# Kernel tuning notes

Measured on AMD Instinct MI355X. Metric: run time of the kernel, lower is better.

## Reference

```python
import jax, jax.numpy as jnp
import numpy as np

B, S, E, H = 4, 2048, 1024, 16
D = E // H
MAX_DIST = 4
LN_EPS = 1e-5


def setup_inputs() -> dict:
    key = jax.random.key(0)
    ks = jax.random.split(key, 12)
    std = 1.0 / np.sqrt(E)
    inp = {
        "x": jax.random.normal(ks[0], (B, S, E), dtype=jnp.float32),
        "distances": jax.random.randint(ks[1], (B, S, S), 0, 5, dtype=jnp.int64),
        "Wq": jax.random.normal(ks[2], (E, E), dtype=jnp.float32) * std,
        "bq": jnp.zeros((E,), dtype=jnp.float32),
        "Wk": jax.random.normal(ks[3], (E, E), dtype=jnp.float32) * std,
        "bk": jnp.zeros((E,), dtype=jnp.float32),
        "Wv": jax.random.normal(ks[4], (E, E), dtype=jnp.float32) * std,
        "bv": jnp.zeros((E,), dtype=jnp.float32),
        "Wo": jax.random.normal(ks[5], (E, E), dtype=jnp.float32) * std,
        "bo": jnp.zeros((E,), dtype=jnp.float32),
        "dist_bias": jax.random.normal(ks[6], (MAX_DIST + 1,), dtype=jnp.float32) * 0.1,
        "ln_g": jnp.ones((E,), dtype=jnp.float32),
        "ln_b": jnp.zeros((E,), dtype=jnp.float32),
    }
    return inp


def _layernorm(y, g, b):
    mu = jnp.mean(y, axis=-1, keepdims=True)
    var = jnp.mean(jnp.square(y - mu), axis=-1, keepdims=True)
    return (y - mu) * jax.lax.rsqrt(var + LN_EPS) * g + b


def reference(x, distances, Wq, bq, Wk, bk, Wv, bv, Wo, bo, dist_bias, ln_g, ln_b):
    scale = 1.0 / np.sqrt(D)
    # projections (torch Linear: x @ W.T + b), split into heads -> [B,H,S,D]
    def heads(y):
        return y.reshape(B, S, H, D).transpose(0, 2, 1, 3)
    q = heads(x @ Wq.T + bq)
    k = heads(x @ Wk.T + bk)
    v = heads(x @ Wv.T + bv)
    scores = jnp.einsum('bhsd,bhtd->bhst', q, k) * scale  # [B,H,S,S]
    d = jnp.clip(distances, 0, MAX_DIST)
    bias = dist_bias[d]  # [B,S,S] gather from learned table
    scores = scores + bias[:, None, :, :]
    attn = jax.nn.softmax(scores, axis=-1)
    out = jnp.einsum('bhst,bhtd->bhsd', attn, v)
    out = out.transpose(0, 2, 1, 3).reshape(B, S, E)
    out = out @ Wo.T + bo
    return _layernorm(x + out, ln_g, ln_b)
```

## Files before the change

kernel.cpp:

```cpp
#include <hip/hip_runtime.h>
#include <stdint.h>

#define NB 4
#define NS 2048
#define NE 1024
#define NH 16
#define ND 64
#define LN_EPS 1e-5f
#define LN2I 1.44269504089f

typedef __attribute__((ext_vector_type(8))) unsigned short u16x8;
typedef __attribute__((ext_vector_type(4))) unsigned short u16x4;
typedef __attribute__((ext_vector_type(8))) short b16x8;
typedef __attribute__((ext_vector_type(4))) float f32x4;
typedef __attribute__((ext_vector_type(16))) float f32x16;
typedef __attribute__((ext_vector_type(4))) unsigned u32x4;

static __device__ __forceinline__ unsigned short f2bf(float f) {
  unsigned u = __builtin_bit_cast(unsigned, f);
  u += 0x7FFFu + ((u >> 16) & 1u);
  return (unsigned short)(u >> 16);
}
static __device__ __forceinline__ float bf2f(unsigned short h) {
  return __builtin_bit_cast(float, (unsigned)h << 16);
}
static __device__ __forceinline__ float bperm_f(int addr, float v) {
  return __builtin_bit_cast(float,
      __builtin_amdgcn_ds_bpermute(addr, __builtin_bit_cast(int, v)));
}
static __device__ __forceinline__ unsigned cvtpk(float lo, float hi) {
  unsigned r;
  asm("v_cvt_pk_bf16_f32 %0, %1, %2" : "=v"(r) : "v"(lo), "v"(hi));
  return r;
}
static __device__ __forceinline__ void plswap(unsigned &a, unsigned &b) {
  asm("v_permlane32_swap_b32 %0, %1" : "+v"(a), "+v"(b));
}
#if __has_builtin(__builtin_amdgcn_exp2f)
static __device__ __forceinline__ float ex2(float x) { return __builtin_amdgcn_exp2f(x); }
#else
static __device__ __forceinline__ float ex2(float x) { return exp2f(x); }
#endif

static __device__ __forceinline__ void gload16(const unsigned short* gsrc,
                                               unsigned short* ldsbase) {
  __builtin_amdgcn_global_load_lds(
      (__attribute__((address_space(1))) unsigned int*)(uintptr_t)gsrc,
      (__attribute__((address_space(3))) unsigned int*)(uintptr_t)ldsbase,
      16, 0, 0);
}

#define MFMA16(a, b, c) __builtin_amdgcn_mfma_f32_16x16x32_bf16( \
    __builtin_bit_cast(b16x8, a), __builtin_bit_cast(b16x8, b), c, 0, 0, 0)
#define MFMA32(a, b, c) __builtin_amdgcn_mfma_f32_32x32x16_bf16( \
    __builtin_bit_cast(b16x8, a), __builtin_bit_cast(b16x8, b), c, 0, 0, 0)

__global__ void k_cvt(const float* __restrict__ src, unsigned short* __restrict__ dst, int n) {
  int i = (blockIdx.x * 256 + threadIdx.x) * 8;
  if (i >= n) return;
  float4 a = *(const float4*)(src + i);
  float4 b = *(const float4*)(src + i + 4);
  u16x8 o;
  o[0]=f2bf(a.x); o[1]=f2bf(a.y); o[2]=f2bf(a.z); o[3]=f2bf(a.w);
  o[4]=f2bf(b.x); o[5]=f2bf(b.y); o[6]=f2bf(b.z); o[7]=f2bf(b.w);
  *(u16x8*)(dst + i) = o;
}

__global__ void k_cvtw(const float* __restrict__ w0, const float* __restrict__ w1,
                       const float* __restrict__ w2, const float* __restrict__ w3,
                       unsigned short* __restrict__ d0, unsigned short* __restrict__ d1,
                       unsigned short* __restrict__ d2, unsigned short* __restrict__ d3) {
  const int z = blockIdx.y;
  const float* src = (z == 0) ? w0 : (z == 1) ? w1 : (z == 2) ? w2 : w3;
  unsigned short* dst = (z == 0) ? d0 : (z == 1) ? d1 : (z == 2) ? d2 : d3;
  int i = (blockIdx.x * 256 + threadIdx.x) * 8;
  float4 a = *(const float4*)(src + i);
  float4 b = *(const float4*)(src + i + 4);
  u16x8 o;
  o[0]=f2bf(a.x); o[1]=f2bf(a.y); o[2]=f2bf(a.z); o[3]=f2bf(a.w);
  o[4]=f2bf(b.x); o[5]=f2bf(b.y); o[6]=f2bf(b.z); o[7]=f2bf(b.w);
  *(u16x8*)(dst + i) = o;
}

__global__ void k_bias(const int* __restrict__ d, const float* __restrict__ tbl,
                       unsigned short* __restrict__ bias) {
  size_t i = ((size_t)blockIdx.x * 256 + threadIdx.x) * 8;
  int4 a = *(const int4*)(d + i);
  int4 b = *(const int4*)(d + i + 4);
  u16x8 o;
  int v;
  v = a.x; v = v < 0 ? 0 : (v > 4 ? 4 : v); o[0] = f2bf(tbl[v] * LN2I);
  v = a.y; v = v < 0 ? 0 : (v > 4 ? 4 : v); o[1] = f2bf(tbl[v] * LN2I);
  v = a.z; v = v < 0 ? 0 : (v > 4 ? 4 : v); o[2] = f2bf(tbl[v] * LN2I);
  v = a.w; v = v < 0 ? 0 : (v > 4 ? 4 : v); o[3] = f2bf(tbl[v] * LN2I);
  v = b.x; v = v < 0 ? 0 : (v > 4 ? 4 : v); o[4] = f2bf(tbl[v] * LN2I);
  v = b.y; v = v < 0 ? 0 : (v > 4 ? 4 : v); o[5] = f2bf(tbl[v] * LN2I);
  v = b.z; v = v < 0 ? 0 : (v > 4 ? 4 : v); o[6] = f2bf(tbl[v] * LN2I);
  v = b.w; v = v < 0 ? 0 : (v > 4 ? 4 : v); o[7] = f2bf(tbl[v] * LN2I);
  *(u16x8*)(bias + i) = o;
}

__global__ __launch_bounds__(256, 3) void k_qkv(
    const unsigned short* __restrict__ xb,
    const unsigned short* __restrict__ wq, const unsigned short* __restrict__ wk_,
    const unsigned short* __restrict__ wv,
    const float* __restrict__ bq, const float* __restrict__ bk_, const float* __restrict__ bv,
    unsigned short* __restrict__ q, unsigned short* __restrict__ kk,
    unsigned short* __restrict__ vt) {
  __shared__ unsigned short sA[128 * 64];
  __shared__ unsigned short sB[128 * 64];
  const int tid = threadIdx.x;
  const int lane = tid & 63, wid = tid >> 6;
  const int g = lane >> 4, c16 = lane & 15;
  const int wm = wid >> 1, wn = wid & 1;
  const int z = blockIdx.z;
  const unsigned short* w = (z == 0) ? wq : ((z == 1) ? wk_ : wv);
  const float* bias = (z == 0) ? bq : ((z == 1) ? bk_ : bv);
  const int n0 = blockIdx.x * 128, m0 = blockIdx.y * 128;

  f32x4 acc[4][4];
#pragma unroll
  for (int i = 0; i < 4; ++i)
#pragma unroll
    for (int j = 0; j < 4; ++j) acc[i][j] = f32x4{0.f, 0.f, 0.f, 0.f};

  const int crow = lane >> 3, gcol8 = (lane & 7) * 8;

  for (int k0 = 0; k0 < NE; k0 += 64) {
#pragma unroll
    for (int i = 0; i < 4; ++i) {
      int c = wid * 4 + i;
      int row = c * 8 + crow;
      gload16(xb + (size_t)(m0 + row) * NE + k0 + gcol8, &sA[c * 512]);
      gload16(w + (size_t)(n0 + row) * NE + k0 + gcol8, &sB[c * 512]);
    }
    __syncthreads();
#pragma unroll
    for (int dc = 0; dc < 2; ++dc) {
      u16x8 af[4], bf[4];
#pragma unroll
      for (int mt = 0; mt < 4; ++mt)
        af[mt] = *(const u16x8*)(sA + (wm * 64 + mt * 16 + c16) * 64 + dc * 32 + g * 8);
#pragma unroll
      for (int nt = 0; nt < 4; ++nt)
        bf[nt] = *(const u16x8*)(sB + (wn * 64 + nt * 16 + c16) * 64 + dc * 32 + g * 8);
#pragma unroll
      for (int mt = 0; mt < 4; ++mt)
#pragma unroll
        for (int nt = 0; nt < 4; ++nt)
          acc[mt][nt] = MFMA16(af[mt], bf[nt], acc[mt][nt]);
    }
    __syncthreads();
  }

  if (z == 0) {
#pragma unroll
    for (int mt = 0; mt < 4; ++mt)
#pragma unroll
      for (int nt = 0; nt < 4; ++nt) {
        int col = n0 + wn * 64 + nt * 16 + c16;
        float bb = bias[col];
#pragma unroll
        for (int rr = 0; rr < 4; ++rr) {
          int row = m0 + wm * 64 + mt * 16 + g * 4 + rr;
          q[(size_t)row * NE + col] = f2bf(acc[mt][nt][rr] + bb);
        }
      }
  } else if (z == 1) {
#pragma unroll
    for (int mt = 0; mt < 4; ++mt)
#pragma unroll
      for (int nt = 0; nt < 4; ++nt) {
        int col = n0 + wn * 64 + nt * 16 + c16;
        float bb = bias[col];
        int seg = col & ~63, d = col & 63;
#pragma unroll
        for (int rr = 0; rr < 4; ++rr) {
          int row = m0 + wm * 64 + mt * 16 + g * 4 + rr;
          int dsw = (((d >> 3) ^ (row & 7)) << 3) | (d & 7);
          kk[(size_t)row * NE + seg + dsw] = f2bf(acc[mt][nt][rr] + bb);
        }
      }
  } else {
#pragma unroll
    for (int mt = 0; mt < 4; ++mt)
#pragma unroll
      for (int nt = 0; nt < 4; ++nt) {
        int col = n0 + wn * 64 + nt * 16 + c16;
        float bb = bias[col];
        int h = col >> 6, dd = col & 63;
        int grow = m0 + wm * 64 + mt * 16 + g * 4;
        int b = grow >> 11, ss = grow & 2047;
        int ssw = (ss & ~63) | (((((ss >> 3) & 7) ^ (dd & 7)) << 3)) | (ss & 7);
        u16x4 o;
#pragma unroll
        for (int rr = 0; rr < 4; ++rr) o[rr] = f2bf(acc[mt][nt][rr] + bb);
        *(u16x4*)(vt + ((size_t)((b * NH + h) * ND + dd)) * NS + ssw) = o;
      }
  }
}

__global__ __launch_bounds__(256, 4) void k_attn(
    const unsigned short* __restrict__ q, const unsigned short* __restrict__ kk,
    const unsigned short* __restrict__ vt, const unsigned short* __restrict__ bias,
    unsigned short* __restrict__ attn) {
  __shared__ unsigned short sK[2][64 * 64];
  __shared__ unsigned short sV[2][64 * 64];
  const int tid = threadIdx.x, lane = tid & 63, wid = tid >> 6;
  const int c32 = lane & 31, hi = lane >> 5;
  const int flat = blockIdx.x;
  const int kdec = flat >> 3;
  const int h = kdec & 15;
  const int G = (flat & 7) | ((kdec >> 4) << 3);
  const int b = G >> 4, qb = G & 15;
  const int q0 = qb * 128 + wid * 32;
  const size_t qkbase = ((size_t)b * NS) * NE + (size_t)h * ND;
  const size_t vbase = ((size_t)(b * NH + h) * ND) * NS;
  const unsigned short* brow = bias + (size_t)b * NS * NS + (size_t)(q0 + c32) * NS;

  u16x8 qf[4];
#pragma unroll
  for (int dc = 0; dc < 4; ++dc)
    qf[dc] = *(const u16x8*)(q + qkbase + (size_t)(q0 + c32) * NE + dc * 16 + hi * 8);

  f32x16 oa[2];
#pragma unroll
  for (int j = 0; j < 2; ++j)
#pragma unroll
    for (int i = 0; i < 16; ++i) oa[j][i] = 0.f;
  float l = 0.f;

  const int crow = lane >> 3, gcol8 = (lane & 7) * 8;
  const int swz = c32 & 7;

  auto stage = [&](int kt, int ib) {
#pragma unroll
    for (int i = 0; i < 4; ++i) {
      int c = wid * 4 + i;
      if (c < 8)
        gload16(kk + qkbase + (size_t)(kt + c * 8 + crow) * NE + gcol8, &sK[ib][c * 512]);
      else
        gload16(vt + vbase + (size_t)((c - 8) * 8 + crow) * NS + kt + gcol8, &sV[ib][(c - 8) * 512]);
    }
  };

  stage(0, 0);

  for (int kt = 0, it = 0; kt < NS; kt += 64, ++it) {
    __syncthreads();
    if (kt + 64 < NS) stage(kt + 64, (it + 1) & 1);
    const unsigned short* bK = &sK[it & 1][0];
    const unsigned short* bV = &sV[it & 1][0];

#pragma unroll
    for (int ts = 0; ts < 2; ++ts) {
      u16x4 bp[4];
#pragma unroll
      for (int k8 = 0; k8 < 4; ++k8)
        bp[k8] = *(const u16x4*)(brow + kt + ts * 32 + k8 * 8 + 4 * hi);
      f32x16 s;
#pragma unroll
      for (int i = 0; i < 16; ++i) s[i] = 0.f;
      __builtin_amdgcn_s_setprio(1);
#pragma unroll
      for (int dc = 0; dc < 4; ++dc) {
        u16x8 kf = *(const u16x8*)(bK + (ts * 32 + c32) * 64 + (((dc * 2 + hi) ^ swz) << 3));
        s = MFMA32(kf, qf[dc], s);
      }
      __builtin_amdgcn_s_setprio(0);
      float rs = 0.f;
#pragma unroll
      for (int r = 0; r < 16; ++r) {
        float e = ex2(s[r] * (0.125f * LN2I) + bf2f(bp[r >> 2][r & 3]));
        s[r] = e;
        rs += e;
      }
      l += rs;
      unsigned u0 = cvtpk(s[0], s[1]), u1 = cvtpk(s[2], s[3]);
      unsigned u2 = cvtpk(s[4], s[5]), u3 = cvtpk(s[6], s[7]);
      plswap(u0, u2);
      plswap(u1, u3);
      u32x4 pa0 = (u32x4){u0, u1, u2, u3};
      unsigned u4 = cvtpk(s[8], s[9]), u5 = cvtpk(s[10], s[11]);
      unsigned u6 = cvtpk(s[12], s[13]), u7 = cvtpk(s[14], s[15]);
      plswap(u4, u6);
      plswap(u5, u7);
      u32x4 pa1 = (u32x4){u4, u5, u6, u7};
      __builtin_amdgcn_s_setprio(1);
#pragma unroll
      for (int kc2 = 0; kc2 < 2; ++kc2) {
        const int kc = ts * 2 + kc2;
        const u32x4 pak = kc2 ? pa1 : pa0;
#pragma unroll
        for (int dcol = 0; dcol < 2; ++dcol) {
          u16x8 vf = *(const u16x8*)(bV + (dcol * 32 + c32) * 64 + (((kc * 2 + hi) ^ swz) << 3));
          oa[dcol] = MFMA32(pak, vf, oa[dcol]);
        }
      }
      __builtin_amdgcn_s_setprio(0);
    }
  }

  float lt = l + __shfl_xor(l, 32);
  float invl = 1.0f / lt;
#pragma unroll
  for (int r = 0; r < 16; ++r) {
    int qrow = (r & 3) + 8 * (r >> 2) + 4 * hi;
    float inv_r = bperm_f(qrow << 2, invl);
#pragma unroll
    for (int dcol = 0; dcol < 2; ++dcol)
      attn[qkbase + (size_t)(q0 + qrow) * NE + dcol * 32 + c32] = f2bf(oa[dcol][r] * inv_r);
  }
}

__global__ __launch_bounds__(256, 3) void k_proj(
    const unsigned short* __restrict__ a, const unsigned short* __restrict__ w,
    const float* __restrict__ bo, const float* __restrict__ x, float* __restrict__ y) {
  __shared__ unsigned short sA[128 * 64];
  __shared__ unsigned short sB[128 * 64];
  const int tid = threadIdx.x;
  const int lane = tid & 63, wid = tid >> 6;
  const int g = lane >> 4, c16 = lane & 15;
  const int wm = wid >> 1, wn = wid & 1;
  const int n0 = blockIdx.x * 128, m0 = blockIdx.y * 128;

  f32x4 acc[4][4];
#pragma unroll
  for (int i = 0; i < 4; ++i)
#pragma unroll
    for (int j = 0; j < 4; ++j) acc[i][j] = f32x4{0.f, 0.f, 0.f, 0.f};

  const int crow = lane >> 3, gcol8 = (lane & 7) * 8;

  for (int k0 = 0; k0 < NE; k0 += 64) {
#pragma unroll
    for (int i = 0; i < 4; ++i) {
      int c = wid * 4 + i;
      int row = c * 8 + crow;
      gload16(a + (size_t)(m0 + row) * NE + k0 + gcol8, &sA[c * 512]);
      gload16(w + (size_t)(n0 + row) * NE + k0 + gcol8, &sB[c * 512]);
    }
    __syncthreads();
#pragma unroll
    for (int dc = 0; dc < 2; ++dc) {
      u16x8 af[4], bf[4];
#pragma unroll
      for (int mt = 0; mt < 4; ++mt)
        af[mt] = *(const u16x8*)(sA + (wm * 64 + mt * 16 + c16) * 64 + dc * 32 + g * 8);
#pragma unroll
      for (int nt = 0; nt < 4; ++nt)
        bf[nt] = *(const u16x8*)(sB + (wn * 64 + nt * 16 + c16) * 64 + dc * 32 + g * 8);
#pragma unroll
      for (int mt = 0; mt < 4; ++mt)
#pragma unroll
        for (int nt = 0; nt < 4; ++nt)
          acc[mt][nt] = MFMA16(af[mt], bf[nt], acc[mt][nt]);
    }
    __syncthreads();
  }

#pragma unroll
  for (int mt = 0; mt < 4; ++mt)
#pragma unroll
    for (int nt = 0; nt < 4; ++nt) {
      int col = n0 + wn * 64 + nt * 16 + c16;
      float bb = bo[col];
#pragma unroll
      for (int rr = 0; rr < 4; ++rr) {
        int row = m0 + wm * 64 + mt * 16 + g * 4 + rr;
        y[(size_t)row * NE + col] = acc[mt][nt][rr] + bb + x[(size_t)row * NE + col];
      }
    }
}

__global__ void k_ln(const float* __restrict__ y, const float* __restrict__ gg,
                     const float* __restrict__ bb, float* __restrict__ out) {
  const int row = blockIdx.x, tid = threadIdx.x;
  float4 v = *(const float4*)(y + (size_t)row * NE + tid * 4);
  float s = v.x + v.y + v.z + v.w;
  float s2 = v.x * v.x + v.y * v.y + v.z * v.z + v.w * v.w;
#pragma unroll
  for (int off = 1; off < 64; off <<= 1) {
    s += __shfl_xor(s, off);
    s2 += __shfl_xor(s2, off);
  }
  __shared__ float red[8];
  const int wid = tid >> 6, lane = tid & 63;
  if (lane == 0) { red[wid * 2] = s; red[wid * 2 + 1] = s2; }
  __syncthreads();
  s = red[0] + red[2] + red[4] + red[6];
  s2 = red[1] + red[3] + red[5] + red[7];
  float mu = s * (1.0f / NE);
  float var = s2 * (1.0f / NE) - mu * mu;
  float rstd = rsqrtf(var + LN_EPS);
  float4 g4 = *(const float4*)(gg + tid * 4);
  float4 b4 = *(const float4*)(bb + tid * 4);
  float4 o;
  o.x = (v.x - mu) * rstd * g4.x + b4.x;
  o.y = (v.y - mu) * rstd * g4.y + b4.y;
  o.z = (v.z - mu) * rstd * g4.z + b4.z;
  o.w = (v.w - mu) * rstd * g4.w + b4.w;
  *(float4*)(out + (size_t)row * NE + tid * 4) = o;
}

extern "C" void kernel_launch(void* const* d_in, const int* in_sizes, int n_in,
                              void* d_out, int out_size, void* d_ws, size_t ws_size,
                              hipStream_t stream) {
  (void)in_sizes; (void)n_in; (void)out_size; (void)ws_size;
  const float* x = (const float*)d_in[0];
  const int* dist = (const int*)d_in[1];
  const float* Wq = (const float*)d_in[2];
  const float* bq = (const float*)d_in[3];
  const float* Wk = (const float*)d_in[4];
  const float* bk = (const float*)d_in[5];
  const float* Wv = (const float*)d_in[6];
  const float* bv = (const float*)d_in[7];
  const float* Wo = (const float*)d_in[8];
  const float* bo = (const float*)d_in[9];
  const float* tbl = (const float*)d_in[10];
  const float* lng = (const float*)d_in[11];
  const float* lnb = (const float*)d_in[12];
  float* out = (float*)d_out;

  char* ws = (char*)d_ws;
  size_t off = 0;
  auto alloc = [&](size_t bytes) {
    char* p = ws + off;
    off += (bytes + 255) & ~(size_t)255;
    return p;
  };
  unsigned short* xb = (unsigned short*)d_out;
  unsigned short* wqb = (unsigned short*)alloc((size_t)NE * NE * 2);
  unsigned short* wkb = (unsigned short*)alloc((size_t)NE * NE * 2);
  unsigned short* wvb = (unsigned short*)alloc((size_t)NE * NE * 2);
  unsigned short* wob = (unsigned short*)alloc((size_t)NE * NE * 2);
  unsigned short* qq  = (unsigned short*)alloc((size_t)NB * NS * NE * 2);
  unsigned short* kb  = (unsigned short*)alloc((size_t)NB * NS * NE * 2);
  unsigned short* vtb = (unsigned short*)alloc((size_t)NB * NS * NE * 2);
  unsigned short* attn = (unsigned short*)alloc((size_t)NB * NS * NE * 2);
  unsigned short* bias = (unsigned short*)alloc((size_t)NB * NS * NS * 2);
  float* y = out;

  k_cvt<<<NB * NS * NE / 2048, 256, 0, stream>>>(x, xb, NB * NS * NE);
  k_cvtw<<<dim3(NE * NE / 2048, 4), 256, 0, stream>>>(Wq, Wk, Wv, Wo, wqb, wkb, wvb, wob);
  k_bias<<<(NB * NS * NS) / 2048, 256, 0, stream>>>(dist, tbl, bias);
  k_qkv<<<dim3(NE / 128, NB * NS / 128, 3), 256, 0, stream>>>(
      xb, wqb, wkb, wvb, bq, bk, bv, qq, kb, vtb);
  k_attn<<<dim3(NB * (NS / 128) * NH), 256, 0, stream>>>(qq, kb, vtb, bias, attn);
  k_proj<<<dim3(NE / 128, NB * NS / 128), 256, 0, stream>>>(attn, wob, bo, x, y);
  k_ln<<<NB * NS, 256, 0, stream>>>(y, lng, lnb, out);
}
```

Before: 330.5 us.

## Restructure attention inner loop to batch QK MFMAs and prefetch bias tiles

The attention kernel now computes both 32-key score tiles back to back before the softmax. It software-pipelines the global bias loads: the next tile's first half is prefetched into registers during the current iteration, and the second half is loaded early. The PV MFMAs are merged into one loop of four steps. Launch bounds drop from 4 to 3 waves per SIMD to make room for the extra live registers, which trades occupancy for more instruction-level overlap of MFMA, exp and global-load latency.

Result: faster. 315.9 us (-4.4%).

```diff
diff --git a/kernel.cpp b/kernel.cpp
--- a/kernel.cpp
+++ b/kernel.cpp
@@ -200,7 +200,7 @@
   }
 }
 
-__global__ __launch_bounds__(256, 4) void k_attn(
+__global__ __launch_bounds__(256, 3) void k_attn(
     const unsigned short* __restrict__ q, const unsigned short* __restrict__ kk,
     const unsigned short* __restrict__ vt, const unsigned short* __restrict__ bias,
     unsigned short* __restrict__ attn) {
@@ -223,11 +223,9 @@
   for (int dc = 0; dc < 4; ++dc)
     qf[dc] = *(const u16x8*)(q + qkbase + (size_t)(q0 + c32) * NE + dc * 16 + hi * 8);
 
-  f32x16 oa[2];
-#pragma unroll
-  for (int j = 0; j < 2; ++j)
-#pragma unroll
-    for (int i = 0; i < 16; ++i) oa[j][i] = 0.f;
+  f32x16 oa0, oa1;
+#pragma unroll
+  for (int i = 0; i < 16; ++i) { oa0[i] = 0.f; oa1[i] = 0.f; }
   float l = 0.f;
 
   const int crow = lane >> 3, gcol8 = (lane & 7) * 8;
@@ -244,7 +242,11 @@
     }
   };
 
+  u16x4 bp0[4], bp1[4];
   stage(0, 0);
+#pragma unroll
+  for (int k8 = 0; k8 < 4; ++k8)
+    bp0[k8] = *(const u16x4*)(brow + k8 * 8 + 4 * hi);
 
   for (int kt = 0, it = 0; kt < NS; kt += 64, ++it) {
     __syncthreads();
@@ -253,52 +255,76 @@
     const unsigned short* bV = &sV[it & 1][0];
 
 #pragma unroll
-    for (int ts = 0; ts < 2; ++ts) {
-      u16x4 bp[4];
+    for (int k8 = 0; k8 < 4; ++k8)
+      bp1[k8] = *(const u16x4*)(brow + kt + 32 + k8 * 8 + 4 * hi);
+
+    f32x16 s0, s1;
+#pragma unroll
+    for (int i = 0; i < 16; ++i) { s0[i] = 0.f; s1[i] = 0.f; }
+    __builtin_amdgcn_s_setprio(1);
+#pragma unroll
+    for (int dc = 0; dc < 4; ++dc) {
+      u16x8 kf = *(const u16x8*)(bK + c32 * 64 + (((dc * 2 + hi) ^ swz) << 3));
+      s0 = MFMA32(kf, qf[dc], s0);
+    }
+#pragma unroll
+    for (int dc = 0; dc < 4; ++dc) {
+      u16x8 kf = *(const u16x8*)(bK + (32 + c32) * 64 + (((dc * 2 + hi) ^ swz) << 3));
+      s1 = MFMA32(kf, qf[dc], s1);
+    }
+    __builtin_amdgcn_s_setprio(0);
+
+    float rs = 0.f;
+#pragma unroll
+    for (int r = 0; r < 16; ++r) {
+      float e = ex2(s0[r] * (0.125f * LN2I) + bf2f(bp0[r >> 2][r & 3]));
+      s0[r] = e;
+      rs += e;
+    }
+    l += rs;
+    unsigned u0 = cvtpk(s0[0], s0[1]), u1 = cvtpk(s0[2], s0[3]);
+    unsigned u2 = cvtpk(s0[4], s0[5]), u3 = cvtpk(s0[6], s0[7]);
+    plswap(u0, u2); plswap(u1, u3);
+    u32x4 pa0 = (u32x4){u0, u1, u2, u3};
+    unsigned u4 = cvtpk(s0[8], s0[9]), u5 = cvtpk(s0[10], s0[11]);
+    unsigned u6 = cvtpk(s0[12], s0[13]), u7 = cvtpk(s0[14], s0[15]);
+    plswap(u4, u6); plswap(u5, u7);
+    u32x4 pa1 = (u32x4){u4, u5, u6, u7};
+
+    if (kt + 64 < NS) {
 #pragma unroll
       for (int k8 = 0; k8 < 4; ++k8)
-        bp[k8] = *(const u16x4*)(brow + kt + ts * 32 + k8 * 8 + 4 * hi);
-      f32x16 s;
-#pragma unroll
-      for (int i = 0; i < 16; ++i) s[i] = 0.f;
-      __builtin_amdgcn_s_setprio(1);
-#pragma unroll
-      for (int dc = 0; dc < 4; ++dc) {
-        u16x8 kf = *(const u16x8*)(bK + (ts * 32 + c32) * 64 + (((dc * 2 + hi) ^ swz) << 3));
-        s = MFMA32(kf, qf[dc], s);
-      }
-      __builtin_amdgcn_s_setprio(0);
-      float rs = 0.f;
-#pragma unroll
-      for (int r = 0; r < 16; ++r) {
-        float e = ex2(s[r] * (0.125f * LN2I) + bf2f(bp[r >> 2][r & 3]));
-        s[r] = e;
-        rs += e;
-      }
-      l += rs;
-      unsigned u0 = cvtpk(s[0], s[1]), u1 = cvtpk(s[2], s[3]);
-      unsigned u2 = cvtpk(s[4], s[5]), u3 = cvtpk(s[6], s[7]);
-      plswap(u0, u2);
-      plswap(u1, u3);
-      u32x4 pa0 = (u32x4){u0, u1, u2, u3};
-      unsigned u4 = cvtpk(s[8], s[9]), u5 = cvtpk(s[10], s[11]);
-      unsigned u6 = cvtpk(s[12], s[13]), u7 = cvtpk(s[14], s[15]);
-      plswap(u4, u6);
-      plswap(u5, u7);
-      u32x4 pa1 = (u32x4){u4, u5, u6, u7};
-      __builtin_amdgcn_s_setprio(1);
-#pragma unroll
-      for (int kc2 = 0; kc2 < 2; ++kc2) {
-        const int kc = ts * 2 + kc2;
-        const u32x4 pak = kc2 ? pa1 : pa0;
-#pragma unroll
-        for (int dcol = 0; dcol < 2; ++dcol) {
-          u16x8 vf = *(const u16x8*)(bV + (dcol * 32 + c32) * 64 + (((kc * 2 + hi) ^ swz) << 3));
-          oa[dcol] = MFMA32(pak, vf, oa[dcol]);
-        }
-      }
-      __builtin_amdgcn_s_setprio(0);
-    }
+        bp0[k8] = *(const u16x4*)(brow + kt + 64 + k8 * 8 + 4 * hi);
+    }
+
+    rs = 0.f;
+#pragma unroll
+    for (int r = 0; r < 16; ++r) {
+      float e = ex2(s1[r] * (0.125f * LN2I) + bf2f(bp1[r >> 2][r & 3]));
+      s1[r] = e;
+      rs += e;
+    }
+    l += rs;
+    u0 = cvtpk(s1[0], s1[1]); u1 = cvtpk(s1[2], s1[3]);
+    u2 = cvtpk(s1[4], s1[5]); u3 = cvtpk(s1[6], s1[7]);
+    plswap(u0, u2); plswap(u1, u3);
+    u32x4 pa2 = (u32x4){u0, u1, u2, u3};
+    u4 = cvtpk(s1[8], s1[9]); u5 = cvtpk(s1[10], s1[11]);
+    u6 = cvtpk(s1[12], s1[13]); u7 = cvtpk(s1[14], s1[15]);
+    plswap(u4, u6); plswap(u5, u7);
+    u32x4 pa3 = (u32x4){u4, u5, u6, u7};
+
+    __builtin_amdgcn_s_setprio(1);
+#pragma unroll
+    for (int kc = 0; kc < 4; ++kc) {
+      const u32x4 pak = (kc == 0) ? pa0 : (kc == 1) ? pa1 : (kc == 2) ? pa2 : pa3;
+      const int gsl = ((kc * 2 + hi) ^ swz) << 3;
+      u16x8 vf0 = *(const u16x8*)(bV + c32 * 64 + gsl);
+      u16x8 vf1 = *(const u16x8*)(bV + (32 + c32) * 64 + gsl);
+      oa0 = MFMA32(pak, vf0, oa0);
+      oa1 = MFMA32(pak, vf1, oa1);
+    }
+    __builtin_amdgcn_s_setprio(0);
   }
 
   float lt = l + __shfl_xor(l, 32);
@@ -307,9 +333,8 @@
   for (int r = 0; r < 16; ++r) {
     int qrow = (r & 3) + 8 * (r >> 2) + 4 * hi;
     float inv_r = bperm_f(qrow << 2, invl);
-#pragma unroll
-    for (int dcol = 0; dcol < 2; ++dcol)
-      attn[qkbase + (size_t)(q0 + qrow) * NE + dcol * 32 + c32] = f2bf(oa[dcol][r] * inv_r);
+    attn[qkbase + (size_t)(q0 + qrow) * NE + c32] = f2bf(oa0[r] * inv_r);
+    attn[qkbase + (size_t)(q0 + qrow) * NE + 32 + c32] = f2bf(oa1[r] * inv_r);
   }
 }
 
```

## Enlarge attention blocks to 512 threads, prefetch bias, compute row sums via MFMA

Applied to the files above, without the earlier changes.

The attention kernel now runs 8 waves per block covering 256 query rows, so each staged K/V tile in LDS is shared by twice as many waves, and the grid shrinks to match. Distance-bias fragments are double-buffered in registers and prefetched one half-tile ahead to hide global load latency. The softmax denominator is now accumulated with extra MFMAs against a ones vector rather than a scalar add chain plus cross-lane shuffles. The MFMA row sum is taken from bf16-rounded probabilities, which changes numerics slightly, and the larger block may lower occupancy flexibility.

Result: faster. 322.6 us (-2.4%).

```diff
diff --git a/kernel.cpp b/kernel.cpp
--- a/kernel.cpp
+++ b/kernel.cpp
@@ -23,10 +23,6 @@
 }
 static __device__ __forceinline__ float bf2f(unsigned short h) {
   return __builtin_bit_cast(float, (unsigned)h << 16);
-}
-static __device__ __forceinline__ float bperm_f(int addr, float v) {
-  return __builtin_bit_cast(float,
-      __builtin_amdgcn_ds_bpermute(addr, __builtin_bit_cast(int, v)));
 }
 static __device__ __forceinline__ unsigned cvtpk(float lo, float hi) {
   unsigned r;
@@ -200,7 +196,7 @@
   }
 }
 
-__global__ __launch_bounds__(256, 4) void k_attn(
+__global__ __launch_bounds__(512, 2) void k_attn(
     const unsigned short* __restrict__ q, const unsigned short* __restrict__ kk,
     const unsigned short* __restrict__ vt, const unsigned short* __restrict__ bias,
     unsigned short* __restrict__ attn) {
@@ -212,8 +208,8 @@
   const int kdec = flat >> 3;
   const int h = kdec & 15;
   const int G = (flat & 7) | ((kdec >> 4) << 3);
-  const int b = G >> 4, qb = G & 15;
-  const int q0 = qb * 128 + wid * 32;
+  const int b = G >> 3, qb = G & 7;
+  const int q0 = qb * 256 + wid * 32;
   const size_t qkbase = ((size_t)b * NS) * NE + (size_t)h * ND;
   const size_t vbase = ((size_t)(b * NH + h) * ND) * NS;
   const unsigned short* brow = bias + (size_t)b * NS * NS + (size_t)(q0 + c32) * NS;
@@ -223,20 +219,21 @@
   for (int dc = 0; dc < 4; ++dc)
     qf[dc] = *(const u16x8*)(q + qkbase + (size_t)(q0 + c32) * NE + dc * 16 + hi * 8);
 
-  f32x16 oa[2];
-#pragma unroll
-  for (int j = 0; j < 2; ++j)
-#pragma unroll
-    for (int i = 0; i < 16; ++i) oa[j][i] = 0.f;
-  float l = 0.f;
+  u16x8 onesv;
+#pragma unroll
+  for (int i = 0; i < 8; ++i) onesv[i] = 0x3F80;
+
+  f32x16 oa[2], l_acc;
+#pragma unroll
+  for (int i = 0; i < 16; ++i) { oa[0][i] = 0.f; oa[1][i] = 0.f; l_acc[i] = 0.f; }
 
   const int crow = lane >> 3, gcol8 = (lane & 7) * 8;
   const int swz = c32 & 7;
 
   auto stage = [&](int kt, int ib) {
 #pragma unroll
-    for (int i = 0; i < 4; ++i) {
-      int c = wid * 4 + i;
+    for (int i = 0; i < 2; ++i) {
+      int c = wid * 2 + i;
       if (c < 8)
         gload16(kk + qkbase + (size_t)(kt + c * 8 + crow) * NE + gcol8, &sK[ib][c * 512]);
       else
@@ -244,7 +241,11 @@
     }
   };
 
+  u16x4 bp[2][4];
   stage(0, 0);
+#pragma unroll
+  for (int k8 = 0; k8 < 4; ++k8)
+    bp[0][k8] = *(const u16x4*)(brow + k8 * 8 + 4 * hi);
 
   for (int kt = 0, it = 0; kt < NS; kt += 64, ++it) {
     __syncthreads();
@@ -254,10 +255,15 @@
 
 #pragma unroll
     for (int ts = 0; ts < 2; ++ts) {
-      u16x4 bp[4];
-#pragma unroll
-      for (int k8 = 0; k8 < 4; ++k8)
-        bp[k8] = *(const u16x4*)(brow + kt + ts * 32 + k8 * 8 + 4 * hi);
+      if (ts == 0) {
+#pragma unroll
+        for (int k8 = 0; k8 < 4; ++k8)
+          bp[1][k8] = *(const u16x4*)(brow + kt + 32 + k8 * 8 + 4 * hi);
+      } else if (kt + 64 < NS) {
+#pragma unroll
+        for (int k8 = 0; k8 < 4; ++k8)
+          bp[0][k8] = *(const u16x4*)(brow + kt + 64 + k8 * 8 + 4 * hi);
+      }
       f32x16 s;
 #pragma unroll
       for (int i = 0; i < 16; ++i) s[i] = 0.f;
@@ -268,25 +274,20 @@
         s = MFMA32(kf, qf[dc], s);
       }
       __builtin_amdgcn_s_setprio(0);
-      float rs = 0.f;
-#pragma unroll
-      for (int r = 0; r < 16; ++r) {
-        float e = ex2(s[r] * (0.125f * LN2I) + bf2f(bp[r >> 2][r & 3]));
-        s[r] = e;
-        rs += e;
-      }
-      l += rs;
+#pragma unroll
+      for (int r = 0; r < 16; ++r)
+        s[r] = ex2(s[r] * (0.125f * LN2I) + bf2f(bp[ts][r >> 2][r & 3]));
       unsigned u0 = cvtpk(s[0], s[1]), u1 = cvtpk(s[2], s[3]);
       unsigned u2 = cvtpk(s[4], s[5]), u3 = cvtpk(s[6], s[7]);
-      plswap(u0, u2);
-      plswap(u1, u3);
+      plswap(u0, u2); plswap(u1, u3);
       u32x4 pa0 = (u32x4){u0, u1, u2, u3};
       unsigned u4 = cvtpk(s[8], s[9]), u5 = cvtpk(s[10], s[11]);
       unsigned u6 = cvtpk(s[12], s[13]), u7 = cvtpk(s[14], s[15]);
-      plswap(u4, u6);
-      plswap(u5, u7);
+      plswap(u4, u6); plswap(u5, u7);
       u32x4 pa1 = (u32x4){u4, u5, u6, u7};
       __builtin_amdgcn_s_setprio(1);
+      l_acc = MFMA32(pa0, onesv, l_acc);
+      l_acc = MFMA32(pa1, onesv, l_acc);
 #pragma unroll
       for (int kc2 = 0; kc2 < 2; ++kc2) {
         const int kc = ts * 2 + kc2;
@@ -301,15 +302,12 @@
     }
   }
 
-  float lt = l + __shfl_xor(l, 32);
-  float invl = 1.0f / lt;
 #pragma unroll
   for (int r = 0; r < 16; ++r) {
     int qrow = (r & 3) + 8 * (r >> 2) + 4 * hi;
-    float inv_r = bperm_f(qrow << 2, invl);
-#pragma unroll
-    for (int dcol = 0; dcol < 2; ++dcol)
-      attn[qkbase + (size_t)(q0 + qrow) * NE + dcol * 32 + c32] = f2bf(oa[dcol][r] * inv_r);
+    float inv_r = 1.0f / l_acc[r];
+    attn[qkbase + (size_t)(q0 + qrow) * NE + c32] = f2bf(oa[0][r] * inv_r);
+    attn[qkbase + (size_t)(q0 + qrow) * NE + 32 + c32] = f2bf(oa[1][r] * inv_r);
   }
 }
 
@@ -446,7 +444,7 @@
   k_bias<<<(NB * NS * NS) / 2048, 256, 0, stream>>>(dist, tbl, bias);
   k_qkv<<<dim3(NE / 128, NB * NS / 128, 3), 256, 0, stream>>>(
       xb, wqb, wkb, wvb, bq, bk, bv, qq, kb, vtb);
-  k_attn<<<dim3(NB * (NS / 128) * NH), 256, 0, stream>>>(qq, kb, vtb, bias, attn);
+  k_attn<<<dim3(NB * (NS / 256) * NH), 512, 0, stream>>>(qq, kb, vtb, bias, attn);
   k_proj<<<dim3(NE / 128, NB * NS / 128), 256, 0, stream>>>(attn, wob, bo, x, y);
   k_ln<<<NB * NS, 256, 0, stream>>>(y, lng, lnb, out);
 }
```
